# Performance work log

Hardware: AMD Instinct MI355X
Metric: run time of the kernel (lower is better)

Reference implementation:

```python
import jax, jax.numpy as jnp
import numpy as np

V, E, EH, H = 32000, 512, 1024, 512  # vocab, emb_dim, enc_hidden, dec_hidden
B, S = 16, 128


def setup_inputs() -> dict:
    key = jax.random.key(0)
    ks = jax.random.split(key, 8)
    g = lambda k, shape, scale: (jax.random.normal(k, shape, jnp.float32) * scale)
    return {
        "y": jax.random.randint(ks[0], (B, S), 0, V),
        "hn": jax.random.normal(ks[1], (B, 1, EH), jnp.float32),
        "emb": g(ks[2], (V, E), 0.02),          # embedding table
        "W_ih": g(ks[3], (3 * H, E), 0.05),      # GRU input weights (r,z,n)
        "W_hh": g(ks[4], (3 * H, H), 0.05),      # GRU hidden weights (r,z,n)
        "b_ih": jnp.zeros((3 * H,), jnp.float32),
        "b_hh": jnp.zeros((3 * H,), jnp.float32),
        "fc_w": g(ks[5], (H, EH), 0.03),         # fc: enc_hidden -> dec_hidden
        "fc_b": jnp.zeros((H,), jnp.float32),
        "pred_w": g(ks[6], (V, H), 0.03),        # pred: dec_hidden -> vocab
        "pred_b": jnp.zeros((V,), jnp.float32),
    }


def gru_scan(x, h0, W_ih, W_hh, b_ih, b_hh):
    """Single-layer unidirectional GRU (PyTorch gate order r,z,n).
    x: [B,S,E], h0: [B,H] -> outputs [B,S,H]."""
    h_dim = h0.shape[-1]
    # precompute input projections for all timesteps: [B,S,3H]
    gx = jnp.einsum('bse,ge->bsg', x, W_ih) + b_ih
    Wr, Wz, Wn = W_hh[:h_dim], W_hh[h_dim:2 * h_dim], W_hh[2 * h_dim:]
    br, bz, bn = b_hh[:h_dim], b_hh[h_dim:2 * h_dim], b_hh[2 * h_dim:]

    def step(h, g):
        gr, gz, gn = g[:, :h_dim], g[:, h_dim:2 * h_dim], g[:, 2 * h_dim:]
        r = jax.nn.sigmoid(gr + h @ Wr.T + br)
        z = jax.nn.sigmoid(gz + h @ Wz.T + bz)
        n = jnp.tanh(gn + r * (h @ Wn.T + bn))
        h_new = (1.0 - z) * n + z * h
        return h_new, h_new

    _, outs = jax.lax.scan(step, h0, jnp.swapaxes(gx, 0, 1))  # [S,B,H]
    return jnp.swapaxes(outs, 0, 1)  # [B,S,H]


def reference(y, hn, emb, W_ih, W_hh, b_ih, b_hh, fc_w, fc_b, pred_w, pred_b):
    # hn: [B,1,EH] -> fc -> [B,1,H] -> permute(1,0,2) -> initial hidden [B,H]
    h0 = (hn @ fc_w.T + fc_b)[:, 0, :]
    x = emb[y]  # [B,S,E]; dropout is identity in eval mode
    out = gru_scan(x, h0, W_ih, W_hh, b_ih, b_hh)  # [B,S,H]
    return out @ pred_w.T + pred_b  # [B,S,V]
```

## Files before the change

### kernel.cpp

```cpp
#include <hip/hip_runtime.h>


typedef __attribute__((ext_vector_type(8))) short           bf8_t;
typedef __attribute__((ext_vector_type(8))) unsigned short  us8_t;
typedef __attribute__((ext_vector_type(4))) unsigned short  us4_t;
typedef __attribute__((ext_vector_type(4))) float           f4_t;

__device__ __forceinline__ unsigned short f2bf(float x) {
    unsigned u = __builtin_bit_cast(unsigned, x);
    u += 0x7FFFu + ((u >> 16) & 1u);
    return (unsigned short)(u >> 16);
}
__device__ __forceinline__ float bf2f(unsigned short h) {
    unsigned u = (unsigned)h << 16;
    return __builtin_bit_cast(float, u);
}
__device__ __forceinline__ float sigm(float x) { return 1.0f / (1.0f + __expf(-x)); }

__device__ __forceinline__ void llc_store_f32(float* p, float v) {
    asm volatile("global_store_dword %0, %1, off sc0 sc1" :: "v"(p), "v"(v) : "memory");
}
__device__ __forceinline__ void llc_store_i32(int* p, int v) {
    asm volatile("global_store_dword %0, %1, off sc0 sc1" :: "v"(p), "v"(v) : "memory");
}
__device__ __forceinline__ int llc_poll_i32(const int* p) {
    int r;
    asm volatile("global_load_dword %0, %1, off sc0 sc1\n\t"
                 "s_waitcnt vmcnt(0)"
                 : "=&v"(r) : "v"(p) : "memory");
    return r;
}

__global__ void k_conv(const float* __restrict__ src, unsigned short* __restrict__ dst, int n4) {
    int i = blockIdx.x * blockDim.x + threadIdx.x;
    int stride = gridDim.x * blockDim.x;
    for (; i < n4; i += stride) {
        f4_t v = ((const f4_t*)src)[i];
        us4_t o;
        o[0] = f2bf(v[0]); o[1] = f2bf(v[1]); o[2] = f2bf(v[2]); o[3] = f2bf(v[3]);
        ((us4_t*)dst)[i] = o;
    }
}

__global__ void k_gather(const int* __restrict__ y, const float* __restrict__ emb,
                         unsigned short* __restrict__ xbf) {
    int m = blockIdx.x;
    int row = y[m];
    int t = threadIdx.x;
    f4_t v = ((const f4_t*)(emb + (size_t)row * 512))[t];
    us4_t o;
    o[0] = f2bf(v[0]); o[1] = f2bf(v[1]); o[2] = f2bf(v[2]); o[3] = f2bf(v[3]);
    ((us4_t*)(xbf + (size_t)m * 512))[t] = o;
}

__global__ void k_h0(const float* __restrict__ hn, const float* __restrict__ fc_w,
                     const float* __restrict__ fc_b, float* __restrict__ h0,
                     int* __restrict__ stamps) {
    __shared__ float sh[1024];
    int b = blockIdx.x, t = threadIdx.x;
    if (b == 0 && t < 64) stamps[t] = 0;
    for (int i = t; i < 1024; i += 256) sh[i] = hn[b * 1024 + i];
    __syncthreads();
    int j = t;
    float a0 = fc_b[j], a1 = fc_b[j + 256];
    const float* w0 = fc_w + (size_t)j * 1024;
    const float* w1 = fc_w + (size_t)(j + 256) * 1024;
    #pragma unroll 8
    for (int e = 0; e < 1024; e++) { float he = sh[e]; a0 += he * w0[e]; a1 += he * w1[e]; }
    h0[b * 512 + j] = a0;
    h0[b * 512 + j + 256] = a1;
}

__launch_bounds__(256)
__global__ void k_gemm(const unsigned short* __restrict__ A, const unsigned short* __restrict__ Bt,
                       const float* __restrict__ bias, float* __restrict__ C, int N) {
    __shared__ unsigned short sA[128 * 64];
    __shared__ unsigned short sB[128 * 64];
    const int m0 = blockIdx.y * 128, n0 = blockIdx.x * 128;
    const int tid = threadIdx.x, lane = tid & 63, wave = tid >> 6;
    const int wm = wave >> 1, wn = wave & 1;
    f4_t acc[4][4] = {};
    for (int ks = 0; ks < 8; ks++) {
        const int k0 = ks * 64;
        #pragma unroll
        for (int t = 0; t < 4; t++) {
            int idx = tid + t * 256;
            int row = idx >> 3, slot = idx & 7;
            int sw = ((slot ^ (row & 7)) << 3);
            *(us8_t*)(&sA[row * 64 + sw]) = *(const us8_t*)(A + (size_t)(m0 + row) * 512 + k0 + slot * 8);
            *(us8_t*)(&sB[row * 64 + sw]) = *(const us8_t*)(Bt + (size_t)(n0 + row) * 512 + k0 + slot * 8);
        }
        __syncthreads();
        #pragma unroll
        for (int kk = 0; kk < 2; kk++) {
            bf8_t af[4], bfr[4];
            #pragma unroll
            for (int mi = 0; mi < 4; mi++) {
                int row = wm * 64 + mi * 16 + (lane & 15);
                int slot = (kk * 4 + (lane >> 4)) ^ (row & 7);
                af[mi] = *(const bf8_t*)(&sA[row * 64 + slot * 8]);
            }
            #pragma unroll
            for (int ni = 0; ni < 4; ni++) {
                int row = wn * 64 + ni * 16 + (lane & 15);
                int slot = (kk * 4 + (lane >> 4)) ^ (row & 7);
                bfr[ni] = *(const bf8_t*)(&sB[row * 64 + slot * 8]);
            }
            #pragma unroll
            for (int mi = 0; mi < 4; mi++)
                #pragma unroll
                for (int ni = 0; ni < 4; ni++)
                    acc[mi][ni] = __builtin_amdgcn_mfma_f32_16x16x32_bf16(af[mi], bfr[ni], acc[mi][ni], 0, 0, 0);
        }
        __syncthreads();
    }
    #pragma unroll
    for (int ni = 0; ni < 4; ni++) {
        int col = n0 + wn * 64 + ni * 16 + (lane & 15);
        float bv = bias[col];
        #pragma unroll
        for (int mi = 0; mi < 4; mi++) {
            int rbase = m0 + wm * 64 + mi * 16 + (lane >> 4) * 4;
            #pragma unroll
            for (int r = 0; r < 4; r++)
                C[(size_t)(rbase + r) * N + col] = acc[mi][ni][r] + bv;
        }
    }
}

__launch_bounds__(512, 1)
__global__ void k_rec(const float* __restrict__ W_hh, const float* __restrict__ b_hh,
                      const float* __restrict__ gx, float* __restrict__ hbuf,
                      int* __restrict__ stamps, unsigned short* __restrict__ Hout) {
    const int kb = blockIdx.x;
    const int j0 = kb * 32;
    const int tid = threadIdx.x, lane = tid & 63, wave = tid >> 6;
    __shared__ unsigned short sHi[16 * 512];
    __shared__ unsigned short sLo[16 * 512];
    __shared__ float sPre[96 * 17];

    bf8_t wfrag[16];
    if (wave < 6) {
        const int gate = wave >> 1, sub = wave & 1;
        const int wrow = gate * 512 + j0 + sub * 16 + (lane & 15);
        const f4_t* wp4 = (const f4_t*)(W_hh + (size_t)wrow * 512);
        #pragma unroll
        for (int kk = 0; kk < 16; kk++) {
            f4_t v0 = wp4[kk * 8 + (lane >> 4) * 2];
            f4_t v1 = wp4[kk * 8 + (lane >> 4) * 2 + 1];
            bf8_t f;
            f[0] = (short)f2bf(v0[0]); f[1] = (short)f2bf(v0[1]);
            f[2] = (short)f2bf(v0[2]); f[3] = (short)f2bf(v0[3]);
            f[4] = (short)f2bf(v1[0]); f[5] = (short)f2bf(v1[1]);
            f[6] = (short)f2bf(v1[2]); f[7] = (short)f2bf(v1[3]);
            wfrag[kk] = f;
        }
    }

    const int b_ = tid >> 5, jj = tid & 31;
    const float brv = b_hh[j0 + jj], bzv = b_hh[512 + j0 + jj], bnv = b_hh[1024 + j0 + jj];
    float h_reg = hbuf[b_ * 512 + j0 + jj];

    for (int s = 1; s <= 128; s++) {
        const float* gxp = gx + (size_t)(b_ * 128 + (s - 1)) * 1536 + j0 + jj;
        float gr = gxp[0], gz = gxp[512], gn = gxp[1024];

        {
            const int target = s - 1;
            int spins = 0; bool ok;
            do {
                int st = target;
                if (lane < 16) st = llc_poll_i32(&stamps[lane]);
                ok = (st >= target);
                if (!ok) __builtin_amdgcn_s_sleep(1);
            } while (!__all(ok) && ++spins < (1 << 20));
        }

        const float* hsrc = hbuf + ((s - 1) & 1) * 8192;
        f4_t hv0, hv1, hv2, hv3;
        {
            const float* p0 = hsrc + (size_t)tid * 4;
            const float* p1 = hsrc + (size_t)(tid + 512) * 4;
            const float* p2 = hsrc + (size_t)(tid + 1024) * 4;
            const float* p3 = hsrc + (size_t)(tid + 1536) * 4;
            asm volatile(
                "global_load_dwordx4 %0, %4, off sc0 sc1\n\t"
                "global_load_dwordx4 %1, %5, off sc0 sc1\n\t"
                "global_load_dwordx4 %2, %6, off sc0 sc1\n\t"
                "global_load_dwordx4 %3, %7, off sc0 sc1\n\t"
                "s_waitcnt vmcnt(0)"
                : "=&v"(hv0), "=&v"(hv1), "=&v"(hv2), "=&v"(hv3)
                : "v"(p0), "v"(p1), "v"(p2), "v"(p3)
                : "memory");
        }
        __builtin_amdgcn_sched_barrier(0);

        {
            f4_t hv[4] = {hv0, hv1, hv2, hv3};
            #pragma unroll
            for (int t = 0; t < 4; t++) {
                int idx4 = tid + t * 512;
                int row = idx4 >> 7, c4 = idx4 & 127;
                us4_t hi, lo;
                #pragma unroll
                for (int i = 0; i < 4; i++) {
                    unsigned short h = f2bf(hv[t][i]);
                    hi[i] = h;
                    lo[i] = f2bf(hv[t][i] - bf2f(h));
                }
                int base = row * 512 + (((c4 >> 1) ^ (row & 7)) << 3) + (c4 & 1) * 4;
                *(us4_t*)(&sHi[base]) = hi;
                *(us4_t*)(&sLo[base]) = lo;
            }
        }
        __syncthreads();

        if (wave < 6) {
            f4_t acc = {0.f, 0.f, 0.f, 0.f};
            const int m = lane & 15;
            #pragma unroll
            for (int kk = 0; kk < 16; kk++) {
                int off = m * 512 + (((kk * 4 + (lane >> 4)) ^ (m & 7)) << 3);
                bf8_t ahi = *(const bf8_t*)(&sHi[off]);
                bf8_t alo = *(const bf8_t*)(&sLo[off]);
                acc = __builtin_amdgcn_mfma_f32_16x16x32_bf16(ahi, wfrag[kk], acc, 0, 0, 0);
                acc = __builtin_amdgcn_mfma_f32_16x16x32_bf16(alo, wfrag[kk], acc, 0, 0, 0);
            }
            const int n = wave * 16 + (lane & 15);
            #pragma unroll
            for (int r = 0; r < 4; r++) sPre[n * 17 + (lane >> 4) * 4 + r] = acc[r];
        }
        __syncthreads();

        float r = sigm(gr + sPre[jj * 17 + b_] + brv);
        float z = sigm(gz + sPre[(32 + jj) * 17 + b_] + bzv);
        float nn = tanhf(gn + r * (sPre[(64 + jj) * 17 + b_] + bnv));
        float hnew = (1.f - z) * nn + z * h_reg;
        h_reg = hnew;

        llc_store_f32(&hbuf[(s & 1) * 8192 + b_ * 512 + j0 + jj], hnew);
        asm volatile("s_waitcnt vmcnt(0)" ::: "memory");
        __syncthreads();
        if (tid == 0) llc_store_i32(&stamps[kb], s);
        Hout[(size_t)(b_ * 128 + (s - 1)) * 512 + j0 + jj] = f2bf(hnew);
    }
}

extern "C" void kernel_launch(void* const* d_in, const int* in_sizes, int n_in,
                              void* d_out, int out_size, void* d_ws, size_t ws_size,
                              hipStream_t stream) {
    const int*   y      = (const int*)  d_in[0];
    const float* hn     = (const float*)d_in[1];
    const float* emb    = (const float*)d_in[2];
    const float* W_ih   = (const float*)d_in[3];
    const float* W_hh   = (const float*)d_in[4];
    const float* b_ih   = (const float*)d_in[5];
    const float* b_hh   = (const float*)d_in[6];
    const float* fc_w   = (const float*)d_in[7];
    const float* fc_b   = (const float*)d_in[8];
    const float* pred_w = (const float*)d_in[9];
    const float* pred_b = (const float*)d_in[10];
    float* out = (float*)d_out;

    char* ws = (char*)d_ws;
    size_t off = 0;
    auto alloc = [&](size_t bytes) { void* p = ws + off; off = (off + bytes + 255) & ~(size_t)255; return p; };
    float*          hbuf   = (float*)          alloc(2 * 16 * 512 * 4);
    int*            stamps = (int*)            alloc(256);
    float*          gx     = (float*)          alloc((size_t)2048 * 1536 * 4);
    unsigned short* Hout   = (unsigned short*) alloc((size_t)2048 * 512 * 2);
    unsigned short* xbf    = (unsigned short*) alloc((size_t)2048 * 512 * 2);
    unsigned short* wihbf  = (unsigned short*) alloc((size_t)1536 * 512 * 2);
    unsigned short* pwbf   = (unsigned short*) alloc((size_t)32000 * 512 * 2);
    (void)ws_size; (void)in_sizes; (void)n_in; (void)out_size;

    k_conv  <<<4096, 256, 0, stream>>>(pred_w, pwbf, 32000 * 512 / 4);
    k_conv  <<<512,  256, 0, stream>>>(W_ih,  wihbf, 1536 * 512 / 4);
    k_gather<<<2048, 128, 0, stream>>>(y, emb, xbf);
    k_h0    <<<16,   256, 0, stream>>>(hn, fc_w, fc_b, hbuf, stamps);
    dim3 gG(12, 16);
    k_gemm  <<<gG, 256, 0, stream>>>(xbf, wihbf, b_ih, gx, 1536);
    k_rec   <<<16, 512, 0, stream>>>(W_hh, b_hh, gx, hbuf, stamps, Hout);
    dim3 gP(250, 16);
    k_gemm  <<<gP, 256, 0, stream>>>(Hout, pwbf, pred_b, out, 32000);
}
```

Before: 688.6 us.

## Replace stamp-based grid barrier with sentinel-filled per-step hidden buffers

The recurrence kernel no longer publishes per-block step stamps and polls them before loading the previous hidden state. Each timestep now gets its own hidden-state slice, pre-filled with a NaN sentinel by a new fill kernel, and consumers spin directly on the data loads until no sentinel remains. This removes the store wait, the extra block barrier and the separate stamp round trip on the serial critical path. The cost is a larger workspace buffer, an extra fill launch, and a reliance on the sentinel bit pattern never appearing as a real hidden value and on dword stores becoming visible atomically.

After: 572.5 us. 1.2x faster.

```diff
diff --git a/kernel.cpp b/kernel.cpp
--- a/kernel.cpp
+++ b/kernel.cpp
@@ -5,6 +5,9 @@
 typedef __attribute__((ext_vector_type(8))) unsigned short  us8_t;
 typedef __attribute__((ext_vector_type(4))) unsigned short  us4_t;
 typedef __attribute__((ext_vector_type(4))) float           f4_t;
+typedef __attribute__((ext_vector_type(4))) unsigned int    u4_t;
+
+#define SENT 0xFFFFFFFFu
 
 __device__ __forceinline__ unsigned short f2bf(float x) {
     unsigned u = __builtin_bit_cast(unsigned, x);
@@ -20,15 +23,11 @@
 __device__ __forceinline__ void llc_store_f32(float* p, float v) {
     asm volatile("global_store_dword %0, %1, off sc0 sc1" :: "v"(p), "v"(v) : "memory");
 }
-__device__ __forceinline__ void llc_store_i32(int* p, int v) {
-    asm volatile("global_store_dword %0, %1, off sc0 sc1" :: "v"(p), "v"(v) : "memory");
-}
-__device__ __forceinline__ int llc_poll_i32(const int* p) {
-    int r;
-    asm volatile("global_load_dword %0, %1, off sc0 sc1\n\t"
-                 "s_waitcnt vmcnt(0)"
-                 : "=&v"(r) : "v"(p) : "memory");
-    return r;
+
+__global__ void k_fill(unsigned int* __restrict__ p) {
+    int i = blockIdx.x * blockDim.x + threadIdx.x;
+    u4_t v = {SENT, SENT, SENT, SENT};
+    ((u4_t*)p)[i] = v;
 }
 
 __global__ void k_conv(const float* __restrict__ src, unsigned short* __restrict__ dst, int n4) {
@@ -54,11 +53,9 @@
 }
 
 __global__ void k_h0(const float* __restrict__ hn, const float* __restrict__ fc_w,
-                     const float* __restrict__ fc_b, float* __restrict__ h0,
-                     int* __restrict__ stamps) {
+                     const float* __restrict__ fc_b, float* __restrict__ h0) {
     __shared__ float sh[1024];
     int b = blockIdx.x, t = threadIdx.x;
-    if (b == 0 && t < 64) stamps[t] = 0;
     for (int i = t; i < 1024; i += 256) sh[i] = hn[b * 1024 + i];
     __syncthreads();
     int j = t;
@@ -131,7 +128,7 @@
 __launch_bounds__(512, 1)
 __global__ void k_rec(const float* __restrict__ W_hh, const float* __restrict__ b_hh,
                       const float* __restrict__ gx, float* __restrict__ hbuf,
-                      int* __restrict__ stamps, unsigned short* __restrict__ Hout) {
+                      unsigned short* __restrict__ Hout) {
     const int kb = blockIdx.x;
     const int j0 = kb * 32;
     const int tid = threadIdx.x, lane = tid & 63, wave = tid >> 6;
@@ -165,24 +162,15 @@
         const float* gxp = gx + (size_t)(b_ * 128 + (s - 1)) * 1536 + j0 + jj;
         float gr = gxp[0], gz = gxp[512], gn = gxp[1024];
 
-        {
-            const int target = s - 1;
-            int spins = 0; bool ok;
-            do {
-                int st = target;
-                if (lane < 16) st = llc_poll_i32(&stamps[lane]);
-                ok = (st >= target);
-                if (!ok) __builtin_amdgcn_s_sleep(1);
-            } while (!__all(ok) && ++spins < (1 << 20));
-        }
-
-        const float* hsrc = hbuf + ((s - 1) & 1) * 8192;
+        const float* hsrc = hbuf + (size_t)(s - 1) * 8192;
+        const float* p0 = hsrc + (size_t)tid * 4;
+        const float* p1 = hsrc + (size_t)(tid + 512) * 4;
+        const float* p2 = hsrc + (size_t)(tid + 1024) * 4;
+        const float* p3 = hsrc + (size_t)(tid + 1536) * 4;
         f4_t hv0, hv1, hv2, hv3;
-        {
-            const float* p0 = hsrc + (size_t)tid * 4;
-            const float* p1 = hsrc + (size_t)(tid + 512) * 4;
-            const float* p2 = hsrc + (size_t)(tid + 1024) * 4;
-            const float* p3 = hsrc + (size_t)(tid + 1536) * 4;
+        int spins = 0;
+        bool ok;
+        do {
             asm volatile(
                 "global_load_dwordx4 %0, %4, off sc0 sc1\n\t"
                 "global_load_dwordx4 %1, %5, off sc0 sc1\n\t"
@@ -192,7 +180,15 @@
                 : "=&v"(hv0), "=&v"(hv1), "=&v"(hv2), "=&v"(hv3)
                 : "v"(p0), "v"(p1), "v"(p2), "v"(p3)
                 : "memory");
-        }
+            ok = true;
+            #pragma unroll
+            for (int i = 0; i < 4; i++) {
+                ok = ok && (__builtin_bit_cast(unsigned, hv0[i]) != SENT)
+                        && (__builtin_bit_cast(unsigned, hv1[i]) != SENT)
+                        && (__builtin_bit_cast(unsigned, hv2[i]) != SENT)
+                        && (__builtin_bit_cast(unsigned, hv3[i]) != SENT);
+            }
+        } while (!ok && ++spins < (1 << 20));
         __builtin_amdgcn_sched_barrier(0);
 
         {
@@ -238,10 +234,7 @@
         float hnew = (1.f - z) * nn + z * h_reg;
         h_reg = hnew;
 
-        llc_store_f32(&hbuf[(s & 1) * 8192 + b_ * 512 + j0 + jj], hnew);
-        asm volatile("s_waitcnt vmcnt(0)" ::: "memory");
-        __syncthreads();
-        if (tid == 0) llc_store_i32(&stamps[kb], s);
+        llc_store_f32(&hbuf[(size_t)s * 8192 + b_ * 512 + j0 + jj], hnew);
         Hout[(size_t)(b_ * 128 + (s - 1)) * 512 + j0 + jj] = f2bf(hnew);
     }
 }
@@ -265,8 +258,7 @@
     char* ws = (char*)d_ws;
     size_t off = 0;
     auto alloc = [&](size_t bytes) { void* p = ws + off; off = (off + bytes + 255) & ~(size_t)255; return p; };
-    float*          hbuf   = (float*)          alloc(2 * 16 * 512 * 4);
-    int*            stamps = (int*)            alloc(256);
+    float*          hbuf   = (float*)          alloc((size_t)129 * 8192 * 4);
     float*          gx     = (float*)          alloc((size_t)2048 * 1536 * 4);
     unsigned short* Hout   = (unsigned short*) alloc((size_t)2048 * 512 * 2);
     unsigned short* xbf    = (unsigned short*) alloc((size_t)2048 * 512 * 2);
@@ -274,13 +266,14 @@
     unsigned short* pwbf   = (unsigned short*) alloc((size_t)32000 * 512 * 2);
     (void)ws_size; (void)in_sizes; (void)n_in; (void)out_size;
 
+    k_fill  <<<1032, 256, 0, stream>>>((unsigned int*)hbuf);
     k_conv  <<<4096, 256, 0, stream>>>(pred_w, pwbf, 32000 * 512 / 4);
     k_conv  <<<512,  256, 0, stream>>>(W_ih,  wihbf, 1536 * 512 / 4);
     k_gather<<<2048, 128, 0, stream>>>(y, emb, xbf);
-    k_h0    <<<16,   256, 0, stream>>>(hn, fc_w, fc_b, hbuf, stamps);
+    k_h0    <<<16,   256, 0, stream>>>(hn, fc_w, fc_b, hbuf);
     dim3 gG(12, 16);
     k_gemm  <<<gG, 256, 0, stream>>>(xbf, wihbf, b_ih, gx, 1536);
-    k_rec   <<<16, 512, 0, stream>>>(W_hh, b_hh, gx, hbuf, stamps, Hout);
+    k_rec   <<<16, 512, 0, stream>>>(W_hh, b_hh, gx, hbuf, Hout);
     dim3 gP(250, 16);
     k_gemm  <<<gP, 256, 0, stream>>>(Hout, pwbf, pred_b, out, 32000);
 }
```
